# Kernel tuning notes

Hardware: AMD Instinct MI355X
Metric: run time of the kernel (lower is better)

Reference implementation:

```python
import jax, jax.numpy as jnp
import numpy as np
from jax import lax

BETA = 0.8
THRESHOLD = 1.0
SURROGATE_ALPHA = 4.0  # slope of sigmoid surrogate gradient
EPS = 1e-12            # matches torch F.normalize eps

@jax.custom_vjp
def surrogate_spike(m):
    # forward: hard threshold at THRESHOLD
    return (m >= THRESHOLD).astype(m.dtype)

def _spike_fwd(m):
    return surrogate_spike(m), m

def _spike_bwd(m, g):
    # sigmoid-derivative surrogate gradient around threshold
    s = jax.nn.sigmoid(SURROGATE_ALPHA * (m - THRESHOLD))
    return (g * SURROGATE_ALPHA * s * (1.0 - s),)

surrogate_spike.defvjp(_spike_fwd, _spike_bwd)

def _l2_normalize(x):
    n = jnp.sqrt(jnp.sum(x * x, axis=-1, keepdims=True))
    return x / jnp.maximum(n, EPS)

def setup_inputs() -> dict:
    key = jax.random.key(0)
    k1, k2, k3 = jax.random.split(key, 3)
    B, T, D, F = 4, 2048, 1024, 4096
    mlp_input = jax.random.normal(k1, (B, T, D), dtype=jnp.float32)
    mlp_activation = jax.random.normal(k2, (B, T, F), dtype=jnp.float32)
    W_proj = jax.random.normal(k3, (F, D), dtype=jnp.float32) * (1.0 / np.sqrt(D))
    theta = jnp.ones((F,), dtype=jnp.float32) * THRESHOLD
    return {"mlp_input": mlp_input, "mlp_activation": mlp_activation,
            "W_proj": W_proj, "theta": theta}

def reference(mlp_input, mlp_activation, W_proj, theta):
    B, T, D = mlp_input.shape
    Fdim = W_proj.shape[0]
    # gate_input: (B, T, d_ff) = mlp_input @ W^T
    gate_input = jnp.einsum('btd,fd->btf', mlp_input, W_proj)

    def step(mem, g_t):
        mem = BETA * mem + g_t               # leaky integrate
        spk = surrogate_spike(mem)           # fire
        mem = mem - theta * spk              # soft reset
        return mem, spk

    mem0 = jnp.zeros((B, Fdim), dtype=gate_input.dtype)
    # scan over time: (T, B, d_ff)
    _, spikes = lax.scan(step, mem0, jnp.swapaxes(gate_input, 0, 1))
    lif_gate = jnp.swapaxes(spikes, 0, 1)    # (B, T, d_ff)

    norm_mlp = _l2_normalize(mlp_activation)
    norm_lif = _l2_normalize(lif_gate)
    # cosine similarity of two (already) unit vectors == dot product
    cos = jnp.sum(norm_mlp * norm_lif, axis=-1)
    return 1.0 - jnp.mean(cos)
```

## Files before the change

### kernel.cpp

```cpp
#include <hip/hip_runtime.h>
#include <hip/hip_bf16.h>

typedef unsigned short u16;
typedef unsigned char  u8;
typedef unsigned long long u64;
typedef __attribute__((ext_vector_type(8))) short short8;
typedef __attribute__((ext_vector_type(4))) float f32x4;

#define T_LEN    2048
#define NB       4
#define K_DIM    1024
#define F_DIM    4096
#define M_FULL   (NB * T_LEN)
#define BETA_C   0.8f
#define THRESH_C 1.0f

__device__ static inline u16 f2bf(float f) {
    unsigned u = __float_as_uint(f);
    unsigned r = u + 0x7FFFu + ((u >> 16) & 1u);
    return (u16)(r >> 16);
}

__global__ __launch_bounds__(256) void cvt_bf16_kernel(const float* __restrict__ in,
                                                       u16* __restrict__ out, int n4) {
    int stride = gridDim.x * blockDim.x;
    for (int i = blockIdx.x * blockDim.x + threadIdx.x; i < n4; i += stride) {
        float4 v = ((const float4*)in)[i];
        ushort4 o;
        o.x = f2bf(v.x); o.y = f2bf(v.y); o.z = f2bf(v.z); o.w = f2bf(v.w);
        ((ushort4*)out)[i] = o;
    }
}

__device__ static inline void gload_lds16(const void* g, void* l) {
    __builtin_amdgcn_global_load_lds(
        (const __attribute__((address_space(1))) unsigned int*)g,
        (__attribute__((address_space(3))) unsigned int*)l, 16, 0, 0);
}

#define NT 16

__global__ __launch_bounds__(512, 2) void gemm8_bt_bf16(const u16* __restrict__ A,
                                                        const u16* __restrict__ Bt,
                                                        u16* __restrict__ Cbf) {
    __shared__ __attribute__((aligned(16))) char lbytes[131072];

    const int tid  = threadIdx.x;
    const int lane = tid & 63;
    const int w    = tid >> 6;
    const int wm   = w >> 2;
    const int wn   = w & 3;

    int orig = blockIdx.x;
    int wg   = (orig & 7) * 64 + (orig >> 3);
    const int by = wg >> 4;
    const int bx = wg & 15;
    const int bm = by * 256;
    const int bn = bx * 256;

    int r0, c0, r1, c1;
    {
        int p = tid << 4;
        int q = p ^ (((p >> 9) & 1) << 5);
        r0 = ((q >> 11) << 4) | ((q >> 6) & 15);
        c0 = (((q >> 10) & 1) << 5) | ((q & 63) >> 1);
        p = (tid + 512) << 4;
        q = p ^ (((p >> 9) & 1) << 5);
        r1 = ((q >> 11) << 4) | ((q >> 6) & 15);
        c1 = (((q >> 10) & 1) << 5) | ((q & 63) >> 1);
    }
    const u16* A00 = A  + (size_t)(bm + r0) * K_DIM + c0;
    const u16* A01 = A  + (size_t)(bm + r1) * K_DIM + c1;
    const u16* A10 = A00 + (size_t)128 * K_DIM;
    const u16* A11 = A01 + (size_t)128 * K_DIM;
    const u16* B00 = Bt + (size_t)(bn + r0) * K_DIM + c0;
    const u16* B01 = Bt + (size_t)(bn + r1) * K_DIM + c1;
    const u16* B10 = B00 + (size_t)128 * K_DIM;
    const u16* B11 = B01 + (size_t)128 * K_DIM;

    const int aswz = (lane & 15) * 64 + (((lane >> 4) * 16) ^ ((lane & 8) << 2));

    f32x4 acc[8][4] = {};
    short8 a[4][2], b0[2][2], b1[2][2];

#define STAGE_A(dst, tk)                                           \
    gload_lds16(A00 + (tk), (dst) + tid * 16);                     \
    gload_lds16(A01 + (tk), (dst) + 8192 + tid * 16);              \
    gload_lds16(A10 + (tk), (dst) + 16384 + tid * 16);             \
    gload_lds16(A11 + (tk), (dst) + 24576 + tid * 16);
#define STAGE_B(dst, tk)                                           \
    gload_lds16(B00 + (tk), (dst) + 32768 + tid * 16);             \
    gload_lds16(B01 + (tk), (dst) + 40960 + tid * 16);             \
    gload_lds16(B10 + (tk), (dst) + 49152 + tid * 16);             \
    gload_lds16(B11 + (tk), (dst) + 57344 + tid * 16);

#define LOAD_A(mh)                                                               \
    _Pragma("unroll") for (int mf = 0; mf < 4; ++mf)                             \
    _Pragma("unroll") for (int ks = 0; ks < 2; ++ks)                             \
        a[mf][ks] = *(const short8*)(aptr + ((mh) * 4 + mf) * 2048 + ks * 1024);
#define LOAD_B(nh, BREG)                                                         \
    _Pragma("unroll") for (int nf = 0; nf < 2; ++nf)                             \
    _Pragma("unroll") for (int ks = 0; ks < 2; ++ks)                             \
        BREG[nf][ks] = *(const short8*)(bptr + ((nh) * 2 + nf) * 2048 + ks * 1024);

#define PHASE_MFMA(mh, nh, BREG)                                                 \
    asm volatile("s_waitcnt lgkmcnt(0)" ::: "memory");                           \
    __builtin_amdgcn_sched_barrier(0);                                           \
    __builtin_amdgcn_s_setprio(1);                                               \
    _Pragma("unroll") for (int mf = 0; mf < 4; ++mf)                             \
    _Pragma("unroll") for (int nf = 0; nf < 2; ++nf)                             \
    _Pragma("unroll") for (int ks = 0; ks < 2; ++ks)                             \
        acc[(mh) * 4 + mf][(nh) * 2 + nf] = __builtin_amdgcn_mfma_f32_16x16x32_bf16( \
            a[mf][ks], BREG[nf][ks], acc[(mh) * 4 + mf][(nh) * 2 + nf], 0, 0, 0);    \
    __builtin_amdgcn_s_setprio(0);

    STAGE_A(lbytes, 0);
    STAGE_B(lbytes, 0);
    asm volatile("s_waitcnt vmcnt(0)" ::: "memory");
    __syncthreads();

    for (int t = 0; t < NT; ++t) {
        const int cur = t & 1;
        const char* aptr = lbytes + cur * 65536 + wm * 16384 + aswz;
        const char* bptr = lbytes + cur * 65536 + 32768 + wn * 8192 + aswz;
        char* sdst = lbytes + (cur ^ 1) * 65536;
        const bool st = (t + 1 < NT);
        const int tk = (t + 1) * 64;

        LOAD_A(0);
        LOAD_B(0, b0);
        if (st) { STAGE_A(sdst, tk); }
        asm volatile("s_waitcnt lgkmcnt(8)" ::: "memory");
        __builtin_amdgcn_s_barrier();
        PHASE_MFMA(0, 0, b0);
        __builtin_amdgcn_s_barrier();

        LOAD_B(1, b1);
        if (st) { STAGE_B(sdst, tk); }
        __builtin_amdgcn_s_barrier();
        PHASE_MFMA(0, 1, b1);
        __builtin_amdgcn_s_barrier();

        LOAD_A(1);
        __builtin_amdgcn_s_barrier();
        PHASE_MFMA(1, 0, b0);
        __builtin_amdgcn_s_barrier();

        PHASE_MFMA(1, 1, b1);
        if (st) { asm volatile("s_waitcnt vmcnt(0)" ::: "memory"); }
        __builtin_amdgcn_s_barrier();
    }

    u16* cl = (u16*)lbytes;
    const int r0w = (lane >> 4) * 4;
    const int cw  = lane & 15;
#pragma unroll
    for (int mi = 0; mi < 8; ++mi)
#pragma unroll
        for (int nj = 0; nj < 4; ++nj)
#pragma unroll
            for (int r = 0; r < 4; ++r)
                cl[(wm * 128 + mi * 16 + r0w + r) * 256 + wn * 64 + nj * 16 + cw] =
                    f2bf(acc[mi][nj][r]);
    __syncthreads();
#pragma unroll
    for (int it = 0; it < 16; ++it) {
        int c   = tid + it * 512;
        int row = c >> 5;
        int cb  = (c & 31) * 8;
        *(short8*)&Cbf[(size_t)(bm + row) * F_DIM + bn + cb] =
            *(const short8*)&cl[row * 256 + cb];
    }
#undef STAGE_A
#undef STAGE_B
#undef LOAD_A
#undef LOAD_B
#undef PHASE_MFMA
}

#define LIF_OUT  256
#define LIF_WARM 128

#define LOADG(buf_, g_)                                                      \
    _Pragma("unroll") for (int u = 0; u < 16; ++u)                           \
        buf_[u] = gp[(size_t)((g_) * 16 + u) * F_DIM];

#define COMPG(buf_, g_) {                                                    \
    const bool out_ = (g_) >= wgrp;                                          \
    _Pragma("unroll") for (int u = 0; u < 16; ++u) {                         \
        float gv = __uint_as_float((unsigned)buf_[u] << 16);                 \
        mem = BETA_C * mem + gv;                                             \
        bool spb = (mem >= THRESH_C);                                        \
        u64 mk = __ballot(spb);                                              \
        if (spb) mem -= th;                                                  \
        if (out_ && lane == 0)                                               \
            pk[(size_t)(((g_) - wgrp) * 16 + u) * 64] = mk;                  \
    } }

__global__ __launch_bounds__(256) void lif_kernel(const u16* __restrict__ gate,
                                                  const float* __restrict__ theta,
                                                  u64* __restrict__ packed) {
    const int tid  = threadIdx.x;
    const int lane = tid & 63;
    const int wid  = blockIdx.x * 4 + (tid >> 6);
    const int s    = wid & 7;
    const int fg   = (wid >> 3) & 63;
    const int b    = wid >> 9;
    const int wgrp = s ? (LIF_WARM / 16) : 0;
    const int ng   = wgrp + LIF_OUT / 16;
    const int t0   = s * LIF_OUT - wgrp * 16;

    const float th = theta[fg * 64 + lane];
    const u16* gp = gate + (size_t)(b * T_LEN + t0) * F_DIM + fg * 64 + lane;
    u64* pk = packed + (size_t)(b * T_LEN + s * LIF_OUT) * 64 + fg;

    float mem = 0.0f;
    u16 ga[16], gb[16], gc[16], gd[16];
    LOADG(ga, 0);
    LOADG(gb, 1);
    LOADG(gc, 2);
    for (int g0 = 0; g0 < ng; g0 += 4) {
        LOADG(gd, g0 + 3);
        COMPG(ga, g0);     if (g0 + 4 < ng) { LOADG(ga, g0 + 4); }
        COMPG(gb, g0 + 1); if (g0 + 5 < ng) { LOADG(gb, g0 + 5); }
        COMPG(gc, g0 + 2); if (g0 + 6 < ng) { LOADG(gc, g0 + 6); }
        COMPG(gd, g0 + 3);
    }
}

__global__ __launch_bounds__(256) void row_reduce_kernel(const float* __restrict__ act,
                                                         const u64* __restrict__ packed,
                                                         float* __restrict__ row_cos) {
    int row = blockIdx.x;
    int tid = threadIdx.x;
    const float* a = act + (size_t)row * F_DIM + tid * 16;
    u64 wv = packed[(size_t)row * 64 + (tid >> 2)];
    unsigned bits = (unsigned)((wv >> ((tid & 3) * 16)) & 0xFFFFull);

    float dot = 0.f, a2 = 0.f;
    float cnt = (float)__popc(bits);
#pragma unroll
    for (int q = 0; q < 4; ++q) {
        float4 av = ((const float4*)a)[q];
        dot += ((bits >> (q * 4 + 0)) & 1) ? av.x : 0.f;
        dot += ((bits >> (q * 4 + 1)) & 1) ? av.y : 0.f;
        dot += ((bits >> (q * 4 + 2)) & 1) ? av.z : 0.f;
        dot += ((bits >> (q * 4 + 3)) & 1) ? av.w : 0.f;
        a2  += av.x * av.x + av.y * av.y + av.z * av.z + av.w * av.w;
    }
#pragma unroll
    for (int off = 32; off > 0; off >>= 1) {
        dot += __shfl_down(dot, off);
        a2  += __shfl_down(a2, off);
        cnt += __shfl_down(cnt, off);
    }
    __shared__ float sd[4], sa[4], sc[4];
    int w = tid >> 6, lane = tid & 63;
    if (lane == 0) { sd[w] = dot; sa[w] = a2; sc[w] = cnt; }
    __syncthreads();
    if (tid == 0) {
        float D  = sd[0] + sd[1] + sd[2] + sd[3];
        float A2 = sa[0] + sa[1] + sa[2] + sa[3];
        float Cn = sc[0] + sc[1] + sc[2] + sc[3];
        float na = fmaxf(sqrtf(A2), 1e-12f);
        float ns = fmaxf(sqrtf(Cn), 1e-12f);
        row_cos[row] = D / (na * ns);
    }
}

__global__ __launch_bounds__(256) void final_reduce_kernel(const float* __restrict__ row_cos,
                                                           float* __restrict__ out) {
    int tid = threadIdx.x;
    float sum = 0.f;
    for (int i = tid; i < M_FULL; i += 256) sum += row_cos[i];
#pragma unroll
    for (int off = 32; off > 0; off >>= 1) sum += __shfl_down(sum, off);
    __shared__ float sw[4];
    int w = tid >> 6, lane = tid & 63;
    if (lane == 0) sw[w] = sum;
    __syncthreads();
    if (tid == 0) out[0] = 1.0f - (sw[0] + sw[1] + sw[2] + sw[3]) * (1.0f / (float)M_FULL);
}

extern "C" void kernel_launch(void* const* d_in, const int* in_sizes, int n_in,
                              void* d_out, int out_size, void* d_ws, size_t ws_size,
                              hipStream_t stream) {
    const float* mlp_input = (const float*)d_in[0];
    const float* mlp_act   = (const float*)d_in[1];
    const float* W         = (const float*)d_in[2];
    const float* theta     = (const float*)d_in[3];
    float* out = (float*)d_out;

    char* ws = (char*)d_ws;
    size_t off = 0;
    auto alloc = [&](size_t n) { size_t o = off; off = (off + n + 255) & ~(size_t)255; return o; };

    u16* A_bf     = (u16*)(ws + alloc((size_t)M_FULL * K_DIM * 2));
    u16* W_bf     = (u16*)(ws + alloc((size_t)F_DIM * K_DIM * 2));
    u64* packed   = (u64*)(ws + alloc((size_t)M_FULL * 64 * 8));
    float* rowcos = (float*)(ws + alloc((size_t)M_FULL * 4));
    u16* gate_bf  = (u16*)(ws + alloc((size_t)M_FULL * F_DIM * 2));

    cvt_bf16_kernel<<<2048, 256, 0, stream>>>(mlp_input, A_bf, M_FULL * K_DIM / 4);
    cvt_bf16_kernel<<<1024, 256, 0, stream>>>(W, W_bf, F_DIM * K_DIM / 4);

    gemm8_bt_bf16<<<(M_FULL / 256) * (F_DIM / 256), 512, 0, stream>>>(A_bf, W_bf, gate_bf);

    lif_kernel<<<512, 256, 0, stream>>>(gate_bf, theta, packed);

    row_reduce_kernel<<<M_FULL, 256, 0, stream>>>(mlp_act, packed, rowcos);
    final_reduce_kernel<<<1, 256, 0, stream>>>(rowcos, out);
}
```

Before: 149.6 us.

## Deepen GEMM global-to-LDS prefetch by splitting stages and prefetching two tiles ahead

The GEMM main loop now splits the A/B tile staging into four half-groups and issues them across the four MFMA phases. Part of the tile two steps ahead is loaded into the current buffer once its rows are consumed. Fine-grained vmcnt waits replace the single end-of-iteration drain, and the last two iterations are peeled. The aim is to hide global load latency better and avoid the full vmcnt(0) stall per tile, at the cost of tricky counter bookkeeping and possible LDS hazards.

```diff
diff --git a/kernel.cpp b/kernel.cpp
--- a/kernel.cpp
+++ b/kernel.cpp
@@ -83,16 +83,14 @@
     f32x4 acc[8][4] = {};
     short8 a[4][2], b0[2][2], b1[2][2];
 
-#define STAGE_A(dst, tk)                                           \
-    gload_lds16(A00 + (tk), (dst) + tid * 16);                     \
-    gload_lds16(A01 + (tk), (dst) + 8192 + tid * 16);              \
-    gload_lds16(A10 + (tk), (dst) + 16384 + tid * 16);             \
-    gload_lds16(A11 + (tk), (dst) + 24576 + tid * 16);
-#define STAGE_B(dst, tk)                                           \
-    gload_lds16(B00 + (tk), (dst) + 32768 + tid * 16);             \
-    gload_lds16(B01 + (tk), (dst) + 40960 + tid * 16);             \
-    gload_lds16(B10 + (tk), (dst) + 49152 + tid * 16);             \
-    gload_lds16(B11 + (tk), (dst) + 57344 + tid * 16);
+#define SG_A02(dst, tk) { gload_lds16(A00 + (tk), (dst) + tid * 16);           \
+                          gload_lds16(A10 + (tk), (dst) + 16384 + tid * 16); }
+#define SG_A13(dst, tk) { gload_lds16(A01 + (tk), (dst) + 8192 + tid * 16);    \
+                          gload_lds16(A11 + (tk), (dst) + 24576 + tid * 16); }
+#define SG_B01(dst, tk) { gload_lds16(B00 + (tk), (dst) + 32768 + tid * 16);   \
+                          gload_lds16(B01 + (tk), (dst) + 40960 + tid * 16); }
+#define SG_B23(dst, tk) { gload_lds16(B10 + (tk), (dst) + 49152 + tid * 16);   \
+                          gload_lds16(B11 + (tk), (dst) + 57344 + tid * 16); }
 
 #define LOAD_A(mh)                                                               \
     _Pragma("unroll") for (int mf = 0; mf < 4; ++mf)                             \
@@ -114,41 +112,58 @@
             a[mf][ks], BREG[nf][ks], acc[(mh) * 4 + mf][(nh) * 2 + nf], 0, 0, 0);    \
     __builtin_amdgcn_s_setprio(0);
 
-    STAGE_A(lbytes, 0);
-    STAGE_B(lbytes, 0);
-    asm volatile("s_waitcnt vmcnt(0)" ::: "memory");
+#define TILE_BODY(DO0, DO1, DO2, DO3, W2ASM, W1ASM, DOW1)                        \
+    LOAD_A(0);                                                                   \
+    LOAD_B(0, b0);                                                               \
+    DO0;                                                                         \
+    asm volatile("s_waitcnt lgkmcnt(8)" ::: "memory");                           \
+    __builtin_amdgcn_s_barrier();                                                \
+    PHASE_MFMA(0, 0, b0);                                                        \
+    __builtin_amdgcn_s_barrier();                                                \
+    LOAD_B(1, b1);                                                               \
+    DO1;                                                                         \
+    __builtin_amdgcn_s_barrier();                                                \
+    PHASE_MFMA(0, 1, b1);                                                        \
+    asm volatile(W2ASM ::: "memory");                                            \
+    __builtin_amdgcn_s_barrier();                                                \
+    LOAD_A(1);                                                                   \
+    DO2;                                                                         \
+    __builtin_amdgcn_s_barrier();                                                \
+    PHASE_MFMA(1, 0, b0);                                                        \
+    __builtin_amdgcn_s_barrier();                                                \
+    DO3;                                                                         \
+    PHASE_MFMA(1, 1, b1);                                                        \
+    if (DOW1) { asm volatile(W1ASM ::: "memory"); }                              \
+    __builtin_amdgcn_s_barrier();
+
+    SG_A02(lbytes, 0); SG_B01(lbytes, 0); SG_B23(lbytes, 0); SG_A13(lbytes, 0);
+    SG_A02(lbytes + 65536, 64);
+    asm volatile("s_waitcnt vmcnt(2)" ::: "memory");
     __syncthreads();
 
-    for (int t = 0; t < NT; ++t) {
+    for (int t = 0; t < NT - 2; ++t) {
         const int cur = t & 1;
         const char* aptr = lbytes + cur * 65536 + wm * 16384 + aswz;
         const char* bptr = lbytes + cur * 65536 + 32768 + wn * 8192 + aswz;
-        char* sdst = lbytes + (cur ^ 1) * 65536;
-        const bool st = (t + 1 < NT);
-        const int tk = (t + 1) * 64;
-
-        LOAD_A(0);
-        LOAD_B(0, b0);
-        if (st) { STAGE_A(sdst, tk); }
-        asm volatile("s_waitcnt lgkmcnt(8)" ::: "memory");
-        __builtin_amdgcn_s_barrier();
-        PHASE_MFMA(0, 0, b0);
-        __builtin_amdgcn_s_barrier();
-
-        LOAD_B(1, b1);
-        if (st) { STAGE_B(sdst, tk); }
-        __builtin_amdgcn_s_barrier();
-        PHASE_MFMA(0, 1, b1);
-        __builtin_amdgcn_s_barrier();
-
-        LOAD_A(1);
-        __builtin_amdgcn_s_barrier();
-        PHASE_MFMA(1, 0, b0);
-        __builtin_amdgcn_s_barrier();
-
-        PHASE_MFMA(1, 1, b1);
-        if (st) { asm volatile("s_waitcnt vmcnt(0)" ::: "memory"); }
-        __builtin_amdgcn_s_barrier();
+        char* dN = lbytes + (cur ^ 1) * 65536;
+        char* dC = lbytes + cur * 65536;
+        const int tk1 = (t + 1) * 64;
+        const int tk2 = (t + 2) * 64;
+        TILE_BODY(SG_B01(dN, tk1), SG_B23(dN, tk1), SG_A13(dN, tk1), SG_A02(dC, tk2),
+                  "s_waitcnt vmcnt(6)", "s_waitcnt vmcnt(4)", true);
+    }
+    {
+        const char* aptr = lbytes + 0 * 65536 + wm * 16384 + aswz;
+        const char* bptr = lbytes + 0 * 65536 + 32768 + wn * 8192 + aswz;
+        char* dN = lbytes + 65536;
+        TILE_BODY(SG_B01(dN, 960), SG_B23(dN, 960), SG_A13(dN, 960), ((void)0),
+                  "s_waitcnt vmcnt(6)", "s_waitcnt vmcnt(2)", true);
+    }
+    {
+        const char* aptr = lbytes + 65536 + wm * 16384 + aswz;
+        const char* bptr = lbytes + 65536 + 32768 + wn * 8192 + aswz;
+        TILE_BODY(((void)0), ((void)0), ((void)0), ((void)0),
+                  "s_waitcnt vmcnt(0)", "s_nop 0", false);
     }
 
     u16* cl = (u16*)lbytes;
@@ -171,11 +186,14 @@
         *(short8*)&Cbf[(size_t)(bm + row) * F_DIM + bn + cb] =
             *(const short8*)&cl[row * 256 + cb];
     }
-#undef STAGE_A
-#undef STAGE_B
+#undef SG_A02
+#undef SG_A13
+#undef SG_B01
+#undef SG_B23
 #undef LOAD_A
 #undef LOAD_B
 #undef PHASE_MFMA
+#undef TILE_BODY
 }
 
 #define LIF_OUT  256
```

Result: no change. 148.4 us (-0.7%).
